# Performance work log

Measured on AMD Instinct MI355X. Metric: run time of the kernel, lower is better.

The kernel has to match this reference:

```python
import jax, jax.numpy as jnp
import numpy as np

EMBED_DIM = 1024
HIDDEN = 4 * EMBED_DIM
BATCH, SEQ = 4, 4096
EPS = 1e-5


def setup_inputs() -> dict:
    key = jax.random.key(0)
    k1, k2, k3 = jax.random.split(key, 3)
    x = jax.random.normal(k1, (BATCH, SEQ, EMBED_DIM), dtype=jnp.float32)
    # Kaiming-ish init scale for linear weights
    w1 = jax.random.normal(k2, (HIDDEN, EMBED_DIM), dtype=jnp.float32) * (1.0 / np.sqrt(EMBED_DIM))
    w2 = jax.random.normal(k3, (EMBED_DIM, HIDDEN), dtype=jnp.float32) * (1.0 / np.sqrt(HIDDEN))
    return {"x": x, "w1": w1, "w2": w2}


def _quant_weight(w):
    # BitNet-b1.58 absmean ternary quantization: clip(round(w/s), -1, 1) * s
    s = jnp.clip(jnp.mean(jnp.abs(w)), EPS, None)
    wq = jnp.clip(jnp.round(w / s), -1.0, 1.0) * s
    # straight-through estimator
    return w + jax.lax.stop_gradient(wq - w)


def _quant_act(x):
    # int8 per-token absmax quantization of activations
    scale = 127.0 / jnp.clip(jnp.max(jnp.abs(x), axis=-1, keepdims=True), EPS, None)
    xq = jnp.clip(jnp.round(x * scale), -128.0, 127.0) / scale
    return x + jax.lax.stop_gradient(xq - x)


def _bitlinear(x, w):
    # x: [..., in], w: [out, in] -> [..., out]
    return jnp.einsum('bsi,oi->bso', _quant_act(x), _quant_weight(w))


def reference(x, w1, w2):
    h = jax.nn.gelu(_bitlinear(x, w1), approximate=False)  # nn.GELU default = exact erf
    return _bitlinear(h, w2)  # dropout is identity in eval / p=0
```

## Files before the change

### kernel.cpp

```cpp
#include <hip/hip_runtime.h>
#include <hip/hip_bf16.h>
#include <cstdint>
#include <cmath>

typedef int intx4 __attribute__((ext_vector_type(4)));
typedef short shortx8 __attribute__((ext_vector_type(8)));

#define EPSQ 1e-5f

__device__ __forceinline__ void async16(const void* g, void* l) {
  __builtin_amdgcn_global_load_lds(
      (const __attribute__((address_space(1))) unsigned int*)(uintptr_t)g,
      (__attribute__((address_space(3))) unsigned int*)(unsigned int)(uintptr_t)l,
      16, 0, 0);
}

__device__ __forceinline__ int q8(float v, float scale, float lo, float hi) {
  return (int)fminf(fmaxf(rintf(v * scale), lo), hi);
}

__device__ __forceinline__ float fast_gelu(float y) {
  const float t = y * 0.70710678118654752f;
  const float x = fabsf(t);
  const float u = __builtin_amdgcn_rcpf(__builtin_fmaf(0.3275911f, x, 1.0f));
  float p = __builtin_fmaf(1.061405429f, u, -1.453152027f);
  p = __builtin_fmaf(p, u, 1.421413741f);
  p = __builtin_fmaf(p, u, -0.284496736f);
  p = __builtin_fmaf(p, u, 0.254829592f);
  p = p * u;
  const float e = __expf(-x * x);
  const float erf_abs = __builtin_fmaf(-p, e, 1.0f);
  const float erf_t = copysignf(erf_abs, t);
  return 0.5f * y * (1.0f + erf_t);
}

__global__ void k_init(float* rowmax, double* sums) {
  int i = blockIdx.x * 256 + threadIdx.x;
  if (i < 16384) rowmax[i] = 0.0f;
  if (i < 2) sums[i] = 0.0;
}

__global__ __launch_bounds__(256) void k_absmean2(const float* __restrict__ W1,
                                                  const float* __restrict__ W2,
                                                  double* __restrict__ sums) {
  __shared__ double wsum[4];
  const int tid = threadIdx.x;
  const int which = blockIdx.x >> 11;
  const float* __restrict__ W = which ? W2 : W1;
  const size_t base = ((size_t)(blockIdx.x & 2047) * 256 + tid) * 8;
  float4 a = *(const float4*)(W + base);
  float4 b = *(const float4*)(W + base + 4);
  float s = fabsf(a.x) + fabsf(a.y) + fabsf(a.z) + fabsf(a.w) +
            fabsf(b.x) + fabsf(b.y) + fabsf(b.z) + fabsf(b.w);
  double d = (double)s;
#pragma unroll
  for (int i = 1; i < 64; i <<= 1) d += __shfl_xor(d, i);
  const int lane = tid & 63, wave = tid >> 6;
  if (lane == 0) wsum[wave] = d;
  __syncthreads();
  if (tid == 0) atomicAdd(sums + which, wsum[0] + wsum[1] + wsum[2] + wsum[3]);
}

__global__ __launch_bounds__(256) void k_quantw2(const float* __restrict__ W1,
                                                 const float* __restrict__ W2,
                                                 signed char* __restrict__ W1Q,
                                                 signed char* __restrict__ W2Q,
                                                 const double* __restrict__ sums) {
  const int which = blockIdx.x >> 11;
  const float* __restrict__ W = which ? W2 : W1;
  signed char* __restrict__ WQ = which ? W2Q : W1Q;
  const float s = fmaxf((float)(sums[which] * (1.0 / 4194304.0)), EPSQ);
  const float inv_s = 1.0f / s;
  const size_t base = ((size_t)(blockIdx.x & 2047) * 256 + threadIdx.x) * 8;
  float4 a = *(const float4*)(W + base);
  float4 b = *(const float4*)(W + base + 4);
  float v[8] = {a.x, a.y, a.z, a.w, b.x, b.y, b.z, b.w};
  unsigned int lo = 0, hi = 0;
#pragma unroll
  for (int j = 0; j < 4; ++j) {
    lo |= ((unsigned int)(q8(v[j], inv_s, -1.f, 1.f) & 0xff)) << (8 * j);
    hi |= ((unsigned int)(q8(v[4 + j], inv_s, -1.f, 1.f) & 0xff)) << (8 * j);
  }
  uint2 o; o.x = lo; o.y = hi;
  *(uint2*)(WQ + base) = o;
}

__global__ __launch_bounds__(256) void k_quantx(const float* __restrict__ X,
                                                signed char* __restrict__ XQ,
                                                float* __restrict__ dqx) {
  __shared__ float wmax[4];
  const int row = blockIdx.x, tid = threadIdx.x;
  const size_t base = (size_t)row * 1024 + tid * 4;
  float4 a = *(const float4*)(X + base);
  float m = fmaxf(fmaxf(fabsf(a.x), fabsf(a.y)), fmaxf(fabsf(a.z), fabsf(a.w)));
#pragma unroll
  for (int i = 1; i < 64; i <<= 1) m = fmaxf(m, __shfl_xor(m, i));
  const int lane = tid & 63, wave = tid >> 6;
  if (lane == 0) wmax[wave] = m;
  __syncthreads();
  m = fmaxf(fmaxf(wmax[0], wmax[1]), fmaxf(wmax[2], wmax[3]));
  m = fmaxf(m, EPSQ);
  const float scale = 127.f / m;
  if (tid == 0) dqx[row] = m * (1.f / 127.f);
  unsigned int p = ((unsigned int)(q8(a.x, scale, -128.f, 127.f) & 0xff)) |
                   ((unsigned int)(q8(a.y, scale, -128.f, 127.f) & 0xff) << 8) |
                   ((unsigned int)(q8(a.z, scale, -128.f, 127.f) & 0xff) << 16) |
                   ((unsigned int)(q8(a.w, scale, -128.f, 127.f) & 0xff) << 24);
  *(unsigned int*)(XQ + base) = p;
}

template <int KB>
__device__ __forceinline__ void gemm_mainloop(const signed char* __restrict__ A,
                                              const signed char* __restrict__ B,
                                              int bm, int bn, int tid, char* lds,
                                              intx4 (&acc)[4][4]) {
  const int wave = tid >> 6, lane = tid & 63;
  const int wm = wave >> 1, wn = wave & 1;
  const int kq = lane >> 4, lc = lane & 15;

  size_t ag[4], bg[4];
#pragma unroll
  for (int i = 0; i < 4; ++i) {
    int gidx = i * 256 + tid;
    int r = gidx >> 3, g = gidx & 7;
    int gs = g ^ (r & 7);
    ag[i] = (size_t)(bm * 128 + r) * KB + gs * 16;
    bg[i] = (size_t)(bn * 128 + r) * KB + gs * 16;
  }
  int aoff[2][4], boff[2][4];
#pragma unroll
  for (int ks = 0; ks < 2; ++ks) {
#pragma unroll
    for (int t = 0; t < 4; ++t) {
      int ra = wm * 64 + t * 16 + lc;
      aoff[ks][t] = ra * 128 + (((ks * 4 + kq) ^ (ra & 7)) << 4);
      int rb = wn * 64 + t * 16 + lc;
      boff[ks][t] = 16384 + rb * 128 + (((ks * 4 + kq) ^ (rb & 7)) << 4);
    }
  }
#pragma unroll
  for (int ti = 0; ti < 4; ++ti)
#pragma unroll
    for (int tj = 0; tj < 4; ++tj) {
      intx4 z = {0, 0, 0, 0};
      acc[ti][tj] = z;
    }

  for (int kt = 0; kt < KB / 128; ++kt) {
    __syncthreads();
    const int k0 = kt * 128;
#pragma unroll
    for (int i = 0; i < 4; ++i) {
      async16(A + ag[i] + k0, lds + i * 4096 + wave * 1024);
      async16(B + bg[i] + k0, lds + 16384 + i * 4096 + wave * 1024);
    }
    asm volatile("s_waitcnt vmcnt(0)" ::: "memory");
    __syncthreads();
#pragma unroll
    for (int ks = 0; ks < 2; ++ks) {
      intx4 af[4], bfr[4];
#pragma unroll
      for (int t = 0; t < 4; ++t) af[t] = *(const intx4*)(lds + aoff[ks][t]);
#pragma unroll
      for (int t = 0; t < 4; ++t) bfr[t] = *(const intx4*)(lds + boff[ks][t]);
#pragma unroll
      for (int ti = 0; ti < 4; ++ti)
#pragma unroll
        for (int tj = 0; tj < 4; ++tj)
          acc[ti][tj] =
              __builtin_amdgcn_mfma_i32_16x16x64_i8(af[ti], bfr[tj], acc[ti][tj], 0, 0, 0);
    }
  }
}

__global__ __launch_bounds__(256) void k_gemm1(const signed char* __restrict__ A,
                                               const signed char* __restrict__ B,
                                               const float* __restrict__ dqx,
                                               const double* __restrict__ sums,
                                               short* __restrict__ HS,
                                               float* __restrict__ mblk,
                                               float* __restrict__ rowmax) {
  __shared__ __attribute__((aligned(16))) char lds[32768];
  const int tid = threadIdx.x;
  const int bm = blockIdx.x, bn = blockIdx.y;

  intx4 acc[4][4];
  gemm_mainloop<1024>(A, B, bm, bn, tid, lds, acc);

  const int wave = tid >> 6, lane = tid & 63;
  const int wm = wave >> 1, wn = wave & 1;
  const int kq = lane >> 4, lc = lane & 15;
  const float s1 = fmaxf((float)(sums[0] * (1.0 / 4194304.0)), EPSQ);

  __syncthreads();
  float* smax = (float*)lds;
  if (tid < 128) smax[tid] = 0.0f;
  __syncthreads();

#pragma unroll
  for (int ti = 0; ti < 4; ++ti) {
#pragma unroll
    for (int r = 0; r < 4; ++r) {
      const int lrow = wm * 64 + ti * 16 + kq * 4 + r;
      const int crow = bm * 128 + lrow;
      const float f = s1 * dqx[crow];
      float mx = 0.f;
#pragma unroll
      for (int tj = 0; tj < 4; ++tj) {
        float y = (float)acc[ti][tj][r] * f;
        float h = fast_gelu(y);
        acc[ti][tj][r] = (int)__float_as_uint(h);
        mx = fmaxf(mx, fabsf(h));
      }
      atomicMax((unsigned int*)&smax[lrow], __float_as_uint(mx));
    }
  }
  __syncthreads();
  if (tid < 128) {
    mblk[(size_t)(bm * 128 + tid) * 32 + bn] = smax[tid];
    atomicMax((unsigned int*)&rowmax[bm * 128 + tid], __float_as_uint(smax[tid]));
  }

#pragma unroll
  for (int ti = 0; ti < 4; ++ti) {
#pragma unroll
    for (int r = 0; r < 4; ++r) {
      const int lrow = wm * 64 + ti * 16 + kq * 4 + r;
      const int crow = bm * 128 + lrow;
      const float sc = 32767.0f / fmaxf(smax[lrow], 1e-30f);
#pragma unroll
      for (int tj = 0; tj < 4; ++tj) {
        const int gcol = bn * 128 + wn * 64 + tj * 16 + lc;
        float h = __uint_as_float((unsigned int)acc[ti][tj][r]);
        int v = (int)fminf(fmaxf(rintf(h * sc), -32767.f), 32767.f);
        HS[(size_t)crow * 4096 + gcol] = (short)v;
      }
    }
  }
}

__global__ __launch_bounds__(256) void k_quanth(const short* __restrict__ HS,
                                                const float* __restrict__ mblk,
                                                const float* __restrict__ rowmax,
                                                signed char* __restrict__ HQ) {
  const size_t gid = (size_t)blockIdx.x * 256 + threadIdx.x;
  const size_t base = gid * 8;
  const int row = (int)(base >> 12);
  const int blk = (int)((base >> 7) & 31);
  const float m = fmaxf(rowmax[row], EPSQ);
  const float fb = mblk[(size_t)row * 32 + blk] * (127.0f / 32767.0f) / m;
  shortx8 s = *(const shortx8*)(HS + base);
  unsigned int lo = 0, hi = 0;
#pragma unroll
  for (int j = 0; j < 4; ++j) {
    lo |= ((unsigned int)(q8((float)s[j], fb, -128.f, 127.f) & 0xff)) << (8 * j);
    hi |= ((unsigned int)(q8((float)s[4 + j], fb, -128.f, 127.f) & 0xff)) << (8 * j);
  }
  uint2 o; o.x = lo; o.y = hi;
  *(uint2*)(HQ + base) = o;
}

__global__ __launch_bounds__(256) void k_gemm2(const signed char* __restrict__ A,
                                               const signed char* __restrict__ B,
                                               const float* __restrict__ rowmax,
                                               const double* __restrict__ sums,
                                               float* __restrict__ OUT) {
  __shared__ __attribute__((aligned(16))) char lds[32768];
  const int tid = threadIdx.x;
  const int bm = blockIdx.x, bn = blockIdx.y;

  intx4 acc[4][4];
  gemm_mainloop<4096>(A, B, bm, bn, tid, lds, acc);

  const int wave = tid >> 6, lane = tid & 63;
  const int wm = wave >> 1, wn = wave & 1;
  const int kq = lane >> 4, lc = lane & 15;
  const float s2 = fmaxf((float)(sums[0] * (1.0 / 4194304.0)), EPSQ);
#pragma unroll
  for (int ti = 0; ti < 4; ++ti) {
#pragma unroll
    for (int r = 0; r < 4; ++r) {
      const int crow = bm * 128 + wm * 64 + ti * 16 + kq * 4 + r;
      const float dqh = fmaxf(rowmax[crow], EPSQ) * (1.f / 127.f);
      const float f = s2 * dqh;
#pragma unroll
      for (int tj = 0; tj < 4; ++tj) {
        const int gcol = bn * 128 + wn * 64 + tj * 16 + lc;
        OUT[(size_t)crow * 1024 + gcol] = (float)acc[ti][tj][r] * f;
      }
    }
  }
}

extern "C" void kernel_launch(void* const* d_in, const int* in_sizes, int n_in,
                              void* d_out, int out_size, void* d_ws, size_t ws_size,
                              hipStream_t stream) {
  const float* X  = (const float*)d_in[0];
  const float* W1 = (const float*)d_in[1];
  const float* W2 = (const float*)d_in[2];
  float* OUT = (float*)d_out;

  char* ws = (char*)d_ws;
  signed char* W1Q = (signed char*)(ws);
  signed char* W2Q = (signed char*)(ws + (4u << 20));
  float* DQX       = (float*)(ws + (8u << 20));
  float* ROWMAX    = (float*)(ws + (8u << 20) + 65536);
  double* SUMS     = (double*)(ws + (8u << 20) + 131072);
  float* MBLK      = (float*)(ws + (9u << 20));
  signed char* HQ  = (signed char*)(ws + (11u << 20));
  const size_t fixed = 75u << 20;
  short* HS = (short*)(ws + fixed);

  signed char* XQ = (signed char*)((char*)d_out + 50331648ull);

  int R = 128;
  const int cands[8] = {16384, 8192, 4096, 2048, 1024, 512, 256, 128};
  for (int i = 0; i < 8; ++i) {
    if (fixed + (size_t)cands[i] * 8192ull <= ws_size) { R = cands[i]; break; }
  }

  hipLaunchKernelGGL(k_init, dim3(64), dim3(256), 0, stream, ROWMAX, SUMS);
  hipLaunchKernelGGL(k_absmean2, dim3(4096), dim3(256), 0, stream, W1, W2, SUMS);
  hipLaunchKernelGGL(k_quantw2, dim3(4096), dim3(256), 0, stream, W1, W2, W1Q, W2Q, SUMS);
  hipLaunchKernelGGL(k_quantx, dim3(16384), dim3(256), 0, stream, X, XQ, DQX);

  const int nchunk = 16384 / R;
  for (int c = 0; c < nchunk; ++c) {
    const int row0 = c * R;
    hipLaunchKernelGGL(k_gemm1, dim3(R / 128, 32), dim3(256), 0, stream,
                       XQ + (size_t)row0 * 1024, W1Q, DQX + row0, SUMS,
                       HS, MBLK + (size_t)row0 * 32, ROWMAX + row0);
    hipLaunchKernelGGL(k_quanth, dim3(R * 2), dim3(256), 0, stream,
                       HS, MBLK + (size_t)row0 * 32, ROWMAX + row0,
                       HQ + (size_t)row0 * 4096);
  }
  hipLaunchKernelGGL(k_gemm2, dim3(128, 8), dim3(256), 0, stream,
                     HQ, W2Q, ROWMAX, SUMS + 1, OUT);
}
```

Measured before the change: 452.9 us.

## Use 256x256 GEMM tiles with a 4-stage async LDS pipeline

Both int8 GEMMs move from 128x128 tiles with 256 threads to 256x256 tiles with 512 threads and a 64-wide K step. Global-to-LDS loads now run through a 4-slot, 128KB LDS ring that keeps three stages in flight with partial vmcnt waits, replacing the single-buffer load-wait-compute loop. MFMA sections are raised in priority with setprio. The GELU epilogue reduces the row max across 16 lanes with shuffles before the LDS atomic, and the per-block max bookkeeping is resized to 16 column blocks. The aim is more data reuse per byte loaded and hiding memory latency. The cost is heavy LDS and register use, which limits residency to about one block per CU, and gemm2 has only 256 blocks to fill the device.

```diff
diff --git a/kernel.cpp b/kernel.cpp
--- a/kernel.cpp
+++ b/kernel.cpp
@@ -110,128 +110,148 @@
 }
 
 template <int KB>
-__device__ __forceinline__ void gemm_mainloop(const signed char* __restrict__ A,
-                                              const signed char* __restrict__ B,
-                                              int bm, int bn, int tid, char* lds,
-                                              intx4 (&acc)[4][4]) {
+__device__ __forceinline__ void gemm_mainloop256(const signed char* __restrict__ A,
+                                                 const signed char* __restrict__ B,
+                                                 int bm, int bn, int tid, char* lds,
+                                                 intx4 (&acc)[8][4]) {
   const int wave = tid >> 6, lane = tid & 63;
-  const int wm = wave >> 1, wn = wave & 1;
+  const int wm = wave >> 2, wn = wave & 3;
   const int kq = lane >> 4, lc = lane & 15;
-
-  size_t ag[4], bg[4];
+  constexpr int NT = KB / 64;
+
+  size_t goff[4];
+  int ldsbase[4];
 #pragma unroll
   for (int i = 0; i < 4; ++i) {
-    int gidx = i * 256 + tid;
-    int r = gidx >> 3, g = gidx & 7;
-    int gs = g ^ (r & 7);
-    ag[i] = (size_t)(bm * 128 + r) * KB + gs * 16;
-    bg[i] = (size_t)(bn * 128 + r) * KB + gs * 16;
-  }
-  int aoff[2][4], boff[2][4];
-#pragma unroll
-  for (int ks = 0; ks < 2; ++ks) {
-#pragma unroll
-    for (int t = 0; t < 4; ++t) {
-      int ra = wm * 64 + t * 16 + lc;
-      aoff[ks][t] = ra * 128 + (((ks * 4 + kq) ^ (ra & 7)) << 4);
-      int rb = wn * 64 + t * 16 + lc;
-      boff[ks][t] = 16384 + rb * 128 + (((ks * 4 + kq) ^ (rb & 7)) << 4);
-    }
-  }
-#pragma unroll
-  for (int ti = 0; ti < 4; ++ti)
-#pragma unroll
-    for (int tj = 0; tj < 4; ++tj) {
+    const int n = i * 512 + tid;
+    const int m = n & 1023;
+    const int r = m >> 2, g = m & 3;
+    const int gl = g ^ ((r >> 1) & 3);
+    const int rowbase = ((i < 2) ? bm : bn) * 256 + r;
+    goff[i] = (size_t)rowbase * KB + gl * 16;
+    ldsbase[i] = (i * 512 + wave * 64) * 16;
+  }
+
+  int aoff[8], boff[4];
+#pragma unroll
+  for (int mi = 0; mi < 8; ++mi) {
+    const int r = wm * 128 + mi * 16 + lc;
+    aoff[mi] = r * 64 + ((kq ^ ((r >> 1) & 3)) << 4);
+  }
+#pragma unroll
+  for (int ni = 0; ni < 4; ++ni) {
+    const int r = wn * 64 + ni * 16 + lc;
+    boff[ni] = 16384 + r * 64 + ((kq ^ ((r >> 1) & 3)) << 4);
+  }
+
+#pragma unroll
+  for (int mi = 0; mi < 8; ++mi)
+#pragma unroll
+    for (int ni = 0; ni < 4; ++ni) {
       intx4 z = {0, 0, 0, 0};
-      acc[ti][tj] = z;
-    }
-
-  for (int kt = 0; kt < KB / 128; ++kt) {
-    __syncthreads();
-    const int k0 = kt * 128;
-#pragma unroll
-    for (int i = 0; i < 4; ++i) {
-      async16(A + ag[i] + k0, lds + i * 4096 + wave * 1024);
-      async16(B + bg[i] + k0, lds + 16384 + i * 4096 + wave * 1024);
-    }
-    asm volatile("s_waitcnt vmcnt(0)" ::: "memory");
-    __syncthreads();
-#pragma unroll
-    for (int ks = 0; ks < 2; ++ks) {
-      intx4 af[4], bfr[4];
-#pragma unroll
-      for (int t = 0; t < 4; ++t) af[t] = *(const intx4*)(lds + aoff[ks][t]);
-#pragma unroll
-      for (int t = 0; t < 4; ++t) bfr[t] = *(const intx4*)(lds + boff[ks][t]);
-#pragma unroll
-      for (int ti = 0; ti < 4; ++ti)
-#pragma unroll
-        for (int tj = 0; tj < 4; ++tj)
-          acc[ti][tj] =
-              __builtin_amdgcn_mfma_i32_16x16x64_i8(af[ti], bfr[tj], acc[ti][tj], 0, 0, 0);
-    }
-  }
-}
-
-__global__ __launch_bounds__(256) void k_gemm1(const signed char* __restrict__ A,
-                                               const signed char* __restrict__ B,
-                                               const float* __restrict__ dqx,
-                                               const double* __restrict__ sums,
-                                               short* __restrict__ HS,
-                                               float* __restrict__ mblk,
-                                               float* __restrict__ rowmax) {
-  __shared__ __attribute__((aligned(16))) char lds[32768];
+      acc[mi][ni] = z;
+    }
+
+#pragma unroll
+  for (int t = 0; t < 3; ++t) {
+    char* lslot = lds + (t & 3) * 32768;
+    const size_t k0 = (size_t)t * 64;
+#pragma unroll
+    for (int i = 0; i < 4; ++i)
+      async16(((i < 2) ? A : B) + goff[i] + k0, lslot + ldsbase[i]);
+  }
+
+  for (int t = 0; t < NT; ++t) {
+    if (t + 2 < NT)      asm volatile("s_waitcnt vmcnt(8)" ::: "memory");
+    else if (t + 1 < NT) asm volatile("s_waitcnt vmcnt(4)" ::: "memory");
+    else                 asm volatile("s_waitcnt vmcnt(0)" ::: "memory");
+    __builtin_amdgcn_s_barrier();
+    __builtin_amdgcn_sched_barrier(0);
+    if (t + 3 < NT) {
+      char* lslot = lds + ((t + 3) & 3) * 32768;
+      const size_t k0 = (size_t)(t + 3) * 64;
+#pragma unroll
+      for (int i = 0; i < 4; ++i)
+        async16(((i < 2) ? A : B) + goff[i] + k0, lslot + ldsbase[i]);
+    }
+    char* lslot = lds + (t & 3) * 32768;
+    intx4 af[8], bf[4];
+#pragma unroll
+    for (int mi = 0; mi < 8; ++mi) af[mi] = *(const intx4*)(lslot + aoff[mi]);
+#pragma unroll
+    for (int ni = 0; ni < 4; ++ni) bf[ni] = *(const intx4*)(lslot + boff[ni]);
+    __builtin_amdgcn_s_setprio(1);
+#pragma unroll
+    for (int mi = 0; mi < 8; ++mi)
+#pragma unroll
+      for (int ni = 0; ni < 4; ++ni)
+        acc[mi][ni] =
+            __builtin_amdgcn_mfma_i32_16x16x64_i8(af[mi], bf[ni], acc[mi][ni], 0, 0, 0);
+    __builtin_amdgcn_s_setprio(0);
+  }
+}
+
+__global__ __launch_bounds__(512, 2) void k_gemm1(const signed char* __restrict__ A,
+                                                  const signed char* __restrict__ B,
+                                                  const float* __restrict__ dqx,
+                                                  const double* __restrict__ sums,
+                                                  short* __restrict__ HS,
+                                                  float* __restrict__ mblk,
+                                                  float* __restrict__ rowmax) {
+  __shared__ __attribute__((aligned(16))) char lds[131072];
   const int tid = threadIdx.x;
   const int bm = blockIdx.x, bn = blockIdx.y;
 
-  intx4 acc[4][4];
-  gemm_mainloop<1024>(A, B, bm, bn, tid, lds, acc);
+  intx4 acc[8][4];
+  gemm_mainloop256<1024>(A, B, bm, bn, tid, lds, acc);
 
   const int wave = tid >> 6, lane = tid & 63;
-  const int wm = wave >> 1, wn = wave & 1;
+  const int wm = wave >> 2, wn = wave & 3;
   const int kq = lane >> 4, lc = lane & 15;
   const float s1 = fmaxf((float)(sums[0] * (1.0 / 4194304.0)), EPSQ);
 
   __syncthreads();
   float* smax = (float*)lds;
-  if (tid < 128) smax[tid] = 0.0f;
-  __syncthreads();
-
-#pragma unroll
-  for (int ti = 0; ti < 4; ++ti) {
+  if (tid < 256) smax[tid] = 0.0f;
+  __syncthreads();
+
+#pragma unroll
+  for (int mi = 0; mi < 8; ++mi) {
 #pragma unroll
     for (int r = 0; r < 4; ++r) {
-      const int lrow = wm * 64 + ti * 16 + kq * 4 + r;
-      const int crow = bm * 128 + lrow;
+      const int lrow = wm * 128 + mi * 16 + kq * 4 + r;
+      const int crow = bm * 256 + lrow;
       const float f = s1 * dqx[crow];
       float mx = 0.f;
 #pragma unroll
-      for (int tj = 0; tj < 4; ++tj) {
-        float y = (float)acc[ti][tj][r] * f;
+      for (int ni = 0; ni < 4; ++ni) {
+        float y = (float)acc[mi][ni][r] * f;
         float h = fast_gelu(y);
-        acc[ti][tj][r] = (int)__float_as_uint(h);
+        acc[mi][ni][r] = (int)__float_as_uint(h);
         mx = fmaxf(mx, fabsf(h));
       }
-      atomicMax((unsigned int*)&smax[lrow], __float_as_uint(mx));
-    }
-  }
-  __syncthreads();
-  if (tid < 128) {
-    mblk[(size_t)(bm * 128 + tid) * 32 + bn] = smax[tid];
-    atomicMax((unsigned int*)&rowmax[bm * 128 + tid], __float_as_uint(smax[tid]));
-  }
-
-#pragma unroll
-  for (int ti = 0; ti < 4; ++ti) {
+#pragma unroll
+      for (int s = 1; s < 16; s <<= 1) mx = fmaxf(mx, __shfl_xor(mx, s));
+      if (lc == 0) atomicMax((unsigned int*)&smax[lrow], __float_as_uint(mx));
+    }
+  }
+  __syncthreads();
+  if (tid < 256) {
+    mblk[(size_t)(bm * 256 + tid) * 16 + bn] = smax[tid];
+    atomicMax((unsigned int*)&rowmax[bm * 256 + tid], __float_as_uint(smax[tid]));
+  }
+
+#pragma unroll
+  for (int mi = 0; mi < 8; ++mi) {
 #pragma unroll
     for (int r = 0; r < 4; ++r) {
-      const int lrow = wm * 64 + ti * 16 + kq * 4 + r;
-      const int crow = bm * 128 + lrow;
+      const int lrow = wm * 128 + mi * 16 + kq * 4 + r;
+      const int crow = bm * 256 + lrow;
       const float sc = 32767.0f / fmaxf(smax[lrow], 1e-30f);
 #pragma unroll
-      for (int tj = 0; tj < 4; ++tj) {
-        const int gcol = bn * 128 + wn * 64 + tj * 16 + lc;
-        float h = __uint_as_float((unsigned int)acc[ti][tj][r]);
+      for (int ni = 0; ni < 4; ++ni) {
+        const int gcol = bn * 256 + wn * 64 + ni * 16 + lc;
+        float h = __uint_as_float((unsigned int)acc[mi][ni][r]);
         int v = (int)fminf(fmaxf(rintf(h * sc), -32767.f), 32767.f);
         HS[(size_t)crow * 4096 + gcol] = (short)v;
       }
@@ -246,9 +266,9 @@
   const size_t gid = (size_t)blockIdx.x * 256 + threadIdx.x;
   const size_t base = gid * 8;
   const int row = (int)(base >> 12);
-  const int blk = (int)((base >> 7) & 31);
+  const int blk = (int)((base >> 8) & 15);
   const float m = fmaxf(rowmax[row], EPSQ);
-  const float fb = mblk[(size_t)row * 32 + blk] * (127.0f / 32767.0f) / m;
+  const float fb = mblk[(size_t)row * 16 + blk] * (127.0f / 32767.0f) / m;
   shortx8 s = *(const shortx8*)(HS + base);
   unsigned int lo = 0, hi = 0;
 #pragma unroll
@@ -260,33 +280,33 @@
   *(uint2*)(HQ + base) = o;
 }
 
-__global__ __launch_bounds__(256) void k_gemm2(const signed char* __restrict__ A,
-                                               const signed char* __restrict__ B,
-                                               const float* __restrict__ rowmax,
-                                               const double* __restrict__ sums,
-                                               float* __restrict__ OUT) {
-  __shared__ __attribute__((aligned(16))) char lds[32768];
+__global__ __launch_bounds__(512, 2) void k_gemm2(const signed char* __restrict__ A,
+                                                  const signed char* __restrict__ B,
+                                                  const float* __restrict__ rowmax,
+                                                  const double* __restrict__ sums,
+                                                  float* __restrict__ OUT) {
+  __shared__ __attribute__((aligned(16))) char lds[131072];
   const int tid = threadIdx.x;
   const int bm = blockIdx.x, bn = blockIdx.y;
 
-  intx4 acc[4][4];
-  gemm_mainloop<4096>(A, B, bm, bn, tid, lds, acc);
+  intx4 acc[8][4];
+  gemm_mainloop256<4096>(A, B, bm, bn, tid, lds, acc);
 
   const int wave = tid >> 6, lane = tid & 63;
-  const int wm = wave >> 1, wn = wave & 1;
+  const int wm = wave >> 2, wn = wave & 3;
   const int kq = lane >> 4, lc = lane & 15;
   const float s2 = fmaxf((float)(sums[0] * (1.0 / 4194304.0)), EPSQ);
 #pragma unroll
-  for (int ti = 0; ti < 4; ++ti) {
+  for (int mi = 0; mi < 8; ++mi) {
 #pragma unroll
     for (int r = 0; r < 4; ++r) {
-      const int crow = bm * 128 + wm * 64 + ti * 16 + kq * 4 + r;
+      const int crow = bm * 256 + wm * 128 + mi * 16 + kq * 4 + r;
       const float dqh = fmaxf(rowmax[crow], EPSQ) * (1.f / 127.f);
       const float f = s2 * dqh;
 #pragma unroll
-      for (int tj = 0; tj < 4; ++tj) {
-        const int gcol = bn * 128 + wn * 64 + tj * 16 + lc;
-        OUT[(size_t)crow * 1024 + gcol] = (float)acc[ti][tj][r] * f;
+      for (int ni = 0; ni < 4; ++ni) {
+        const int gcol = bn * 256 + wn * 64 + ni * 16 + lc;
+        OUT[(size_t)crow * 1024 + gcol] = (float)acc[mi][ni][r] * f;
       }
     }
   }
@@ -307,15 +327,15 @@
   float* ROWMAX    = (float*)(ws + (8u << 20) + 65536);
   double* SUMS     = (double*)(ws + (8u << 20) + 131072);
   float* MBLK      = (float*)(ws + (9u << 20));
-  signed char* HQ  = (signed char*)(ws + (11u << 20));
-  const size_t fixed = 75u << 20;
+  signed char* HQ  = (signed char*)(ws + (10u << 20));
+  const size_t fixed = 74u << 20;
   short* HS = (short*)(ws + fixed);
 
   signed char* XQ = (signed char*)((char*)d_out + 50331648ull);
 
-  int R = 128;
-  const int cands[8] = {16384, 8192, 4096, 2048, 1024, 512, 256, 128};
-  for (int i = 0; i < 8; ++i) {
+  int R = 256;
+  const int cands[7] = {16384, 8192, 4096, 2048, 1024, 512, 256};
+  for (int i = 0; i < 7; ++i) {
     if (fixed + (size_t)cands[i] * 8192ull <= ws_size) { R = cands[i]; break; }
   }
 
@@ -327,13 +347,13 @@
   const int nchunk = 16384 / R;
   for (int c = 0; c < nchunk; ++c) {
     const int row0 = c * R;
-    hipLaunchKernelGGL(k_gemm1, dim3(R / 128, 32), dim3(256), 0, stream,
+    hipLaunchKernelGGL(k_gemm1, dim3(R / 256, 16), dim3(512), 0, stream,
                        XQ + (size_t)row0 * 1024, W1Q, DQX + row0, SUMS,
-                       HS, MBLK + (size_t)row0 * 32, ROWMAX + row0);
+                       HS, MBLK + (size_t)row0 * 16, ROWMAX + row0);
     hipLaunchKernelGGL(k_quanth, dim3(R * 2), dim3(256), 0, stream,
-                       HS, MBLK + (size_t)row0 * 32, ROWMAX + row0,
+                       HS, MBLK + (size_t)row0 * 16, ROWMAX + row0,
                        HQ + (size_t)row0 * 4096);
   }
-  hipLaunchKernelGGL(k_gemm2, dim3(128, 8), dim3(256), 0, stream,
+  hipLaunchKernelGGL(k_gemm2, dim3(64, 4), dim3(512), 0, stream,
                      HQ, W2Q, ROWMAX, SUMS + 1, OUT);
 }
```

After: 418.5 us. 1.08x faster.
